# Optimization experiments

Measured on AMD Instinct MI355X. Metric: run time of the kernel, lower is better.

The kernel has to match this reference:

```python
import jax, jax.numpy as jnp
import numpy as np

H = 4096
NUM_HEADS = 32
D = 128
SEQ_LEN = 1024
CTX = 4096


def setup_inputs() -> dict:
    key = jax.random.key(0)
    k1, k2, k3, k4 = jax.random.split(key, 4)
    X = jax.random.normal(k1, (SEQ_LEN, H), dtype=jnp.float32)
    # Linear weight [out=3H, in=H]; scale ~1/sqrt(H) so attention logits are O(1)
    W = jax.random.normal(k2, (3 * H, H), dtype=jnp.float32) * (1.0 / np.sqrt(H))
    cache_K = jax.random.normal(k3, (1, CTX, NUM_HEADS, D), dtype=jnp.float32)
    cache_V = jax.random.normal(k4, (1, CTX, NUM_HEADS, D), dtype=jnp.float32)
    return {"X": X, "W": W, "cache_K": cache_K, "cache_V": cache_V}


def reference(X, W, cache_K, cache_V):
    seq_len, h = X.shape
    nh, d = cache_K.shape[2], cache_K.shape[3]
    # fused QKV projection (Linear, no bias): X @ W^T -> [seq_len, 3H]
    qkv = X @ W.T
    q, k, v = jnp.split(qkv, 3, axis=1)
    q = q.reshape(1, seq_len, nh, d)
    k = k.reshape(1, seq_len, nh, d)
    v = v.reshape(1, seq_len, nh, d)
    # concat KV cache along the sequence dim (cache_K[:, :P] with P = full cache)
    k_full = jnp.concatenate([cache_K, k], axis=1)  # [1, ctx+seq, nh, d]
    v_full = jnp.concatenate([cache_V, v], axis=1)
    scale = 1.0 / np.sqrt(d)
    # scores: [1, nh, seq_q, kv_len]
    scores = jnp.einsum("bqhd,bkhd->bhqk", q, k_full) * scale
    weights = jax.nn.softmax(scores, axis=-1)
    out = jnp.einsum("bhqk,bkhd->bqhd", weights, v_full)  # [1, seq, nh, d]
    return out.reshape(seq_len, h)
```

## Files before the change

kernel.cpp:

```cpp
#include <hip/hip_runtime.h>
#include <hip/hip_bf16.h>
#include <stdint.h>

#define H_DIM 4096
#define NH 32
#define HD 128
#define SEQ 1024
#define CTX 4096
#define KVL (CTX + SEQ)
#define W3H (3 * H_DIM)
#define ATTN_SCALE 0.08838834764831845f

typedef short short8 __attribute__((ext_vector_type(8)));
typedef float f32x4 __attribute__((ext_vector_type(4)));

#define GLOAD_LDS16(g, l)                                             \
  __builtin_amdgcn_global_load_lds(                                   \
      (const __attribute__((address_space(1))) void*)(g),             \
      (__attribute__((address_space(3))) void*)(l), 16, 0, 0)

__device__ __forceinline__ unsigned short f2b(float f) {
  union { float f; unsigned u; } v; v.f = f;
  return (unsigned short)((v.u + 0x7FFFu + ((v.u >> 16) & 1u)) >> 16);
}
__device__ __forceinline__ float b2f(unsigned short u) {
  union { unsigned u; float f; } v; v.u = ((unsigned)u) << 16;
  return v.f;
}

__global__ void k_cvt2(const float* __restrict__ X, const float* __restrict__ W,
                       unsigned short* __restrict__ Xb, unsigned short* __restrict__ Wb) {
  const int nx = SEQ * H_DIM / 4;
  const int nw = W3H * H_DIM / 4;
  int i = blockIdx.x * 256 + threadIdx.x;
  const float* s;
  unsigned short* d;
  int j;
  if (i < nx) { s = X; d = Xb; j = i; }
  else { j = i - nx; if (j >= nw) return; s = W; d = Wb; }
  float4 v = reinterpret_cast<const float4*>(s)[j];
  ushort4 o;
  o.x = f2b(v.x); o.y = f2b(v.y); o.z = f2b(v.z); o.w = f2b(v.w);
  reinterpret_cast<ushort4*>(d)[j] = o;
}

#define BM 128
#define BN 128
#define BK 64
__global__ __launch_bounds__(256, 2) void k_gemm_qkv(
    const unsigned short* __restrict__ A,
    const unsigned short* __restrict__ B,
    unsigned short* __restrict__ C) {
  __shared__ unsigned short As[BM * BK];
  __shared__ unsigned short Bs[BN * BK];
  const int tid = threadIdx.x;
  const int lane = tid & 63;
  const int wid = tid >> 6;
  const int bn = blockIdx.x, bm = blockIdx.y;
  const int wr = wid >> 1, wc = wid & 1;

  f32x4 acc[4][4] = {};

  const int lrow = lane >> 3;
  const int lcol = (lane & 7) * 8;
  const unsigned short* ga = A + (size_t)(bm * BM + wid * 32 + lrow) * H_DIM + lcol;
  const unsigned short* gb = B + (size_t)(bn * BN + wid * 32 + lrow) * H_DIM + lcol;

  for (int kt = 0; kt < H_DIM / BK; ++kt) {
    __syncthreads();
    const unsigned short* gak = ga + kt * BK;
    const unsigned short* gbk = gb + kt * BK;
#pragma unroll
    for (int i = 0; i < 4; ++i) {
      GLOAD_LDS16(gak + i * 8 * H_DIM, As + (wid * 4 + i) * 512);
      GLOAD_LDS16(gbk + i * 8 * H_DIM, Bs + (wid * 4 + i) * 512);
    }
    __syncthreads();
#pragma unroll
    for (int kk = 0; kk < 2; ++kk) {
      short8 af[4], bfr[4];
#pragma unroll
      for (int m = 0; m < 4; ++m)
        af[m] = *reinterpret_cast<const short8*>(
            As + (wr * 64 + m * 16 + (lane & 15)) * BK + kk * 32 + (lane >> 4) * 8);
#pragma unroll
      for (int n = 0; n < 4; ++n)
        bfr[n] = *reinterpret_cast<const short8*>(
            Bs + (wc * 64 + n * 16 + (lane & 15)) * BK + kk * 32 + (lane >> 4) * 8);
#pragma unroll
      for (int m = 0; m < 4; ++m)
#pragma unroll
        for (int n = 0; n < 4; ++n)
          acc[m][n] = __builtin_amdgcn_mfma_f32_16x16x32_bf16(af[m], bfr[n], acc[m][n], 0, 0, 0);
    }
  }
  const int r0 = bm * BM + wr * 64 + (lane >> 4) * 4;
  const int c0 = bn * BN + wc * 64 + (lane & 15);
#pragma unroll
  for (int m = 0; m < 4; ++m)
#pragma unroll
    for (int n = 0; n < 4; ++n)
#pragma unroll
      for (int r = 0; r < 4; ++r)
        C[(size_t)(r0 + m * 16 + r) * W3H + c0 + n * 16] = f2b(acc[m][n][r]);
}

__global__ void k_build_k(const float* __restrict__ cK, const unsigned short* __restrict__ QKV,
                          unsigned short* __restrict__ Kb) {
  int idx = (blockIdx.x * 256 + threadIdx.x) * 4;
  if (idx >= NH * KVL * HD) return;
  int h = idx / (KVL * HD);
  int rem = idx % (KVL * HD);
  int kv = rem / HD;
  int d = rem % HD;
  ushort4 o;
  if (kv < CTX) {
    float4 v = *reinterpret_cast<const float4*>(cK + ((size_t)kv * NH + h) * HD + d);
    o.x = f2b(v.x); o.y = f2b(v.y); o.z = f2b(v.z); o.w = f2b(v.w);
  } else {
    o = *reinterpret_cast<const ushort4*>(QKV + (size_t)(kv - CTX) * W3H + H_DIM + h * HD + d);
  }
  *reinterpret_cast<ushort4*>(Kb + idx) = o;
}

__global__ void k_build_vt(const float* __restrict__ cV, const unsigned short* __restrict__ QKV,
                           unsigned short* __restrict__ Vt) {
  __shared__ unsigned short T[HD][66];
  const int h = blockIdx.y;
  const int kt = blockIdx.x;
  const int t = threadIdx.x;
#pragma unroll
  for (int e = 0; e < 8; ++e) {
    int idx = (t + e * 256) * 4;
    int kvl = idx >> 7;
    int d = idx & 127;
    int kv = kt * 64 + kvl;
    unsigned short a, b, c, w;
    if (kv < CTX) {
      float4 v = *reinterpret_cast<const float4*>(cV + ((size_t)kv * NH + h) * HD + d);
      a = f2b(v.x); b = f2b(v.y); c = f2b(v.z); w = f2b(v.w);
    } else {
      ushort4 u = *reinterpret_cast<const ushort4*>(QKV + (size_t)(kv - CTX) * W3H + 2 * H_DIM + h * HD + d);
      a = u.x; b = u.y; c = u.z; w = u.w;
    }
    T[d][kvl] = a; T[d + 1][kvl] = b; T[d + 2][kvl] = c; T[d + 3][kvl] = w;
  }
  __syncthreads();
#pragma unroll
  for (int e = 0; e < 8; ++e) {
    int idx = (t + e * 256) * 4;
    int d = idx >> 6;
    int kv0 = idx & 63;
    ushort4 o;
    o.x = T[d][kv0]; o.y = T[d][kv0 + 1]; o.z = T[d][kv0 + 2]; o.w = T[d][kv0 + 3];
    *reinterpret_cast<ushort4*>(Vt + ((size_t)h * HD + d) * KVL + kt * 64 + kv0) = o;
  }
}

#define KVT 64
#define NT (KVL / KVT)
#define NT2 (NT / 2)
__global__ __launch_bounds__(256, 2) void k_attn(
    const unsigned short* __restrict__ QKV,
    const unsigned short* __restrict__ Kb,
    const unsigned short* __restrict__ Vt,
    float* __restrict__ A0,
    float* __restrict__ A1,
    float* __restrict__ Mp,
    float* __restrict__ Lp) {
  __shared__ unsigned short Ks[2][KVT * HD];
  __shared__ unsigned short Vs[2][KVT * HD];
  const int tid = threadIdx.x, lane = tid & 63, wid = tid >> 6;
  const int g = lane >> 4;
  const int qi = lane & 15;
  const int id = blockIdx.x;
  const int xcd = id & 7, slot = id >> 3;
  const int h = xcd * 4 + (slot >> 4);
  const int rem = slot & 15;
  const int qt = rem >> 1;
  const int split = rem & 1;
  const int kt0 = split * NT2;
  const int q0 = qt * 128 + wid * 32;

  short8 qf[2][4];
#pragma unroll
  for (int hf = 0; hf < 2; ++hf)
#pragma unroll
    for (int c = 0; c < 4; ++c) {
      short8 q = *reinterpret_cast<const short8*>(
          QKV + (size_t)(q0 + hf * 16 + qi) * W3H + h * HD + c * 32 + g * 8);
      short8 t;
#pragma unroll
      for (int j = 0; j < 8; ++j) t[j] = (short)f2b(b2f((unsigned short)q[j]) * ATTN_SCALE);
      qf[hf][c] = t;
    }

  float m_r[2] = {-1e30f, -1e30f}, l_r[2] = {0.f, 0.f};
  f32x4 acc_o[2][8] = {};

  const char* Kh = (const char*)(Kb + (size_t)h * KVL * HD);
  const char* Vh = (const char*)(Vt + (size_t)h * HD * KVL);

#define STAGE_K(t, b)                                                          \
  {                                                                            \
    _Pragma("unroll") for (int i = 0; i < 4; ++i) {                            \
      int c = wid * 4 + i;                                                     \
      int krow = c * 4 + (lane >> 4);                                          \
      int klcb = (16 * (lane & 15)) ^ ((krow & 7) << 4);                       \
      GLOAD_LDS16(Kh + (size_t)((t) * KVT + krow) * 256 + klcb,                \
                  (char*)Ks[b] + c * 1024);                                    \
    }                                                                          \
  }
#define STAGE_V(t, b)                                                          \
  {                                                                            \
    _Pragma("unroll") for (int i = 0; i < 4; ++i) {                            \
      int c = wid * 4 + i;                                                     \
      int vrow = c * 8 + (lane >> 3);                                          \
      int vlcb = (16 * (lane & 7)) ^ ((vrow & 7) << 4);                        \
      GLOAD_LDS16(Vh + (size_t)vrow * (KVL * 2) + (size_t)(t) * 128 + vlcb,    \
                  (char*)Vs[b] + c * 1024);                                    \
    }                                                                          \
  }
#define QKT(buf, S)                                                            \
  {                                                                            \
    _Pragma("unroll") for (int n = 0; n < 4; ++n) {                            \
      S[0][n] = (f32x4){0.f, 0.f, 0.f, 0.f};                                   \
      S[1][n] = (f32x4){0.f, 0.f, 0.f, 0.f};                                   \
    }                                                                          \
    __builtin_amdgcn_s_setprio(1);                                             \
    _Pragma("unroll") for (int n = 0; n < 4; ++n) {                            \
      int row = n * 16 + qi;                                                   \
      _Pragma("unroll") for (int c = 0; c < 4; ++c) {                          \
        int cb = (c * 32 + g * 8) * 2;                                         \
        short8 kf = *reinterpret_cast<const short8*>(                          \
            (const char*)Ks[buf] + row * 256 + (cb ^ ((row & 7) << 4)));       \
        S[0][n] = __builtin_amdgcn_mfma_f32_16x16x32_bf16(kf, qf[0][c], S[0][n], 0, 0, 0); \
        S[1][n] = __builtin_amdgcn_mfma_f32_16x16x32_bf16(kf, qf[1][c], S[1][n], 0, 0, 0); \
      }                                                                        \
    }                                                                          \
    __builtin_amdgcn_s_setprio(0);                                             \
  }

  const int i0 = ((2 * (g & 1) + 0) * 16 + qi) * 4;
  const int i1 = ((2 * (g & 1) + 1) * 16 + qi) * 4;

#define SMPV(S, vb)                                                            \
  {                                                                            \
    float p[2][4][4];                                                          \
    int okv = 1;                                                               \
    float tmax[2];                                                             \
    _Pragma("unroll") for (int hf = 0; hf < 2; ++hf) {                         \
      float t0 = S[hf][0][0];                                                  \
      _Pragma("unroll") for (int n = 0; n < 4; ++n)                            \
        _Pragma("unroll") for (int r = 0; r < 4; ++r)                          \
          t0 = fmaxf(t0, S[hf][n][r]);                                         \
      t0 = fmaxf(t0, __shfl_xor(t0, 16, 64));                                  \
      t0 = fmaxf(t0, __shfl_xor(t0, 32, 64));                                  \
      tmax[hf] = t0;                                                           \
      okv &= (t0 <= m_r[hf] + 8.0f);                                           \
    }                                                                          \
    if (!__all(okv)) {                                                         \
      _Pragma("unroll") for (int hf = 0; hf < 2; ++hf) {                       \
        float mn = fmaxf(m_r[hf], tmax[hf]);                                   \
        float alpha = __expf(m_r[hf] - mn);                                    \
        l_r[hf] *= alpha;                                                      \
        m_r[hf] = mn;                                                          \
        _Pragma("unroll") for (int nd = 0; nd < 8; ++nd) acc_o[hf][nd] *= alpha; \
      }                                                                        \
    }                                                                          \
    _Pragma("unroll") for (int hf = 0; hf < 2; ++hf) {                         \
      float sum = 0.f;                                                         \
      _Pragma("unroll") for (int n = 0; n < 4; ++n)                            \
        _Pragma("unroll") for (int r = 0; r < 4; ++r) {                        \
          p[hf][n][r] = __expf(S[hf][n][r] - m_r[hf]);                         \
          sum += p[hf][n][r];                                                  \
        }                                                                      \
      sum += __shfl_xor(sum, 16, 64);                                          \
      sum += __shfl_xor(sum, 32, 64);                                          \
      l_r[hf] += sum;                                                          \
    }                                                                          \
    unsigned pr[2][4][2];                                                      \
    _Pragma("unroll") for (int hf = 0; hf < 2; ++hf)                           \
      _Pragma("unroll") for (int n = 0; n < 4; ++n)                            \
        _Pragma("unroll") for (int rr = 0; rr < 2; ++rr) {                     \
          union { __hip_bfloat162 b; unsigned u; } cv;                         \
          cv.b = __float22bfloat162_rn(                                        \
              make_float2(p[hf][n][2 * rr], p[hf][n][2 * rr + 1]));            \
          pr[hf][n][rr] = cv.u;                                                \
        }                                                                      \
    _Pragma("unroll") for (int kc = 0; kc < 2; ++kc) {                         \
      short8 pv[2];                                                            \
      _Pragma("unroll") for (int hf = 0; hf < 2; ++hf) {                       \
        int a0 = __builtin_amdgcn_ds_bpermute(i0, (int)pr[hf][2 * kc][0]);     \
        int b0 = __builtin_amdgcn_ds_bpermute(i0, (int)pr[hf][2 * kc + 1][0]); \
        int a1 = __builtin_amdgcn_ds_bpermute(i0, (int)pr[hf][2 * kc][1]);     \
        int b1 = __builtin_amdgcn_ds_bpermute(i0, (int)pr[hf][2 * kc + 1][1]); \
        int a2 = __builtin_amdgcn_ds_bpermute(i1, (int)pr[hf][2 * kc][0]);     \
        int b2 = __builtin_amdgcn_ds_bpermute(i1, (int)pr[hf][2 * kc + 1][0]); \
        int a3 = __builtin_amdgcn_ds_bpermute(i1, (int)pr[hf][2 * kc][1]);     \
        int b3 = __builtin_amdgcn_ds_bpermute(i1, (int)pr[hf][2 * kc + 1][1]); \
        union { int i[4]; short8 s8; } u;                                      \
        u.i[0] = (g < 2) ? a0 : b0;                                            \
        u.i[1] = (g < 2) ? a1 : b1;                                            \
        u.i[2] = (g < 2) ? a2 : b2;                                            \
        u.i[3] = (g < 2) ? a3 : b3;                                            \
        pv[hf] = u.s8;                                                         \
      }                                                                        \
      __builtin_amdgcn_s_setprio(1);                                           \
      _Pragma("unroll") for (int nd = 0; nd < 8; ++nd) {                       \
        int row = nd * 16 + qi;                                                \
        int cb = kc * 64 + g * 16;                                             \
        short8 vf = *reinterpret_cast<const short8*>(                          \
            (const char*)Vs[vb] + row * 128 + (cb ^ ((row & 7) << 4)));        \
        acc_o[0][nd] = __builtin_amdgcn_mfma_f32_16x16x32_bf16(vf, pv[0], acc_o[0][nd], 0, 0, 0); \
        acc_o[1][nd] = __builtin_amdgcn_mfma_f32_16x16x32_bf16(vf, pv[1], acc_o[1][nd], 0, 0, 0); \
      }                                                                        \
      __builtin_amdgcn_s_setprio(0);                                           \
    }                                                                          \
  }

#define BODY(t, SC, SN)                                                        \
  {                                                                            \
    const int cur = (t) & 1;                                                   \
    if ((t) + 2 < NT2) STAGE_K(kt0 + (t) + 2, cur);                            \
    if ((t) + 1 < NT2) QKT(cur ^ 1, SN);                                       \
    SMPV(SC, cur);                                                             \
    __syncthreads();                                                           \
    if ((t) + 2 < NT2) STAGE_V(kt0 + (t) + 2, cur);                            \
  }

  STAGE_K(kt0, 0);
  STAGE_V(kt0, 0);
  STAGE_K(kt0 + 1, 1);
  STAGE_V(kt0 + 1, 1);
  __syncthreads();

  f32x4 sA[2][4], sB[2][4];
  QKT(0, sA);

  for (int tt = 0; tt < NT2; tt += 2) {
    BODY(tt, sA, sB);
    BODY(tt + 1, sB, sA);
  }

  float* Op = split ? A1 : A0;
#pragma unroll
  for (int hf = 0; hf < 2; ++hf) {
    float* orow = Op + (size_t)(q0 + hf * 16 + qi) * H_DIM + h * HD;
#pragma unroll
    for (int nd = 0; nd < 8; ++nd)
      *reinterpret_cast<float4*>(orow + nd * 16 + g * 4) =
          *reinterpret_cast<const float4*>(&acc_o[hf][nd]);
    if (g == 0) {
      int q = q0 + hf * 16 + qi;
      Mp[split * (NH * SEQ) + h * SEQ + q] = m_r[hf];
      Lp[split * (NH * SEQ) + h * SEQ + q] = l_r[hf];
    }
  }
#undef STAGE_K
#undef STAGE_V
#undef QKT
#undef SMPV
#undef BODY
}

__global__ void k_combine(const float* __restrict__ A1, const float* __restrict__ Mp,
                          const float* __restrict__ Lp, float* __restrict__ out) {
  int i4 = blockIdx.x * 256 + threadIdx.x;
  int q = i4 >> 10;
  int c4 = i4 & 1023;
  int h = c4 >> 5;
  float m0 = Mp[h * SEQ + q], m1 = Mp[NH * SEQ + h * SEQ + q];
  float l0 = Lp[h * SEQ + q], l1 = Lp[NH * SEQ + h * SEQ + q];
  float M = fmaxf(m0, m1);
  float w0 = __expf(m0 - M), w1 = __expf(m1 - M);
  float inv = 1.0f / (w0 * l0 + w1 * l1);
  float4 a0 = reinterpret_cast<const float4*>(out)[i4];
  float4 a1 = reinterpret_cast<const float4*>(A1)[i4];
  float4 o;
  o.x = (w0 * a0.x + w1 * a1.x) * inv;
  o.y = (w0 * a0.y + w1 * a1.y) * inv;
  o.z = (w0 * a0.z + w1 * a1.z) * inv;
  o.w = (w0 * a0.w + w1 * a1.w) * inv;
  reinterpret_cast<float4*>(out)[i4] = o;
}

extern "C" void kernel_launch(void* const* d_in, const int* in_sizes, int n_in,
                              void* d_out, int out_size, void* d_ws, size_t ws_size,
                              hipStream_t stream) {
  const float* X = (const float*)d_in[0];
  const float* W = (const float*)d_in[1];
  const float* cK = (const float*)d_in[2];
  const float* cV = (const float*)d_in[3];
  float* out = (float*)d_out;
  char* ws = (char*)d_ws;

  unsigned short* Xb = (unsigned short*)(ws);
  float* Mp = (float*)(ws);
  float* Lp = (float*)(ws + (256 << 10));
  unsigned short* QKVb = (unsigned short*)(ws + ((size_t)8 << 20));
  unsigned short* Wb = (unsigned short*)(ws + ((size_t)32 << 20));
  unsigned short* Kb = (unsigned short*)(ws + ((size_t)32 << 20));
  unsigned short* Vt = (unsigned short*)(ws + ((size_t)72 << 20));
  float* A1 = (float*)(ws + ((size_t)112 << 20));

  int ncvt = (SEQ * H_DIM + W3H * H_DIM) / 4;
  k_cvt2<<<(ncvt + 255) / 256, 256, 0, stream>>>(X, W, Xb, Wb);

  dim3 gg(W3H / BN, SEQ / BM);
  k_gemm_qkv<<<gg, 256, 0, stream>>>(Xb, Wb, QKVb);

  k_build_k<<<(NH * KVL * HD / 4) / 256, 256, 0, stream>>>(cK, QKVb, Kb);
  dim3 gv(KVL / 64, NH);
  k_build_vt<<<gv, 256, 0, stream>>>(cV, QKVb, Vt);

  k_attn<<<SEQ / 128 * NH * 2, 256, 0, stream>>>(QKVb, Kb, Vt, out, A1, Mp, Lp);
  k_combine<<<(SEQ * H_DIM / 4) / 256, 256, 0, stream>>>(A1, Mp, Lp, out);
}
```

Baseline: 354.4 us.

## Rewrite QKV GEMM with 256x256 tiles, double-buffered LDS and XOR swizzle

The QKV projection GEMM moves from 128x128 tiles with a single LDS buffer to 256x256 tiles on 512 threads. It double-buffers 128KB of LDS so global-to-LDS loads of the next k-tiles overlap the MFMA work, and XOR-swizzles the LDS layout to avoid bank conflicts. It also remaps block IDs for L2 locality and raises wave priority around the MFMA bursts. The cost is 192 blocks on a 256-CU part, which leaves some CUs idle, plus heavy LDS use and register pressure from 32 accumulators per thread.

```diff
diff --git a/kernel.cpp b/kernel.cpp
--- a/kernel.cpp
+++ b/kernel.cpp
@@ -44,65 +44,101 @@
   reinterpret_cast<ushort4*>(d)[j] = o;
 }
 
-#define BM 128
-#define BN 128
-#define BK 64
-__global__ __launch_bounds__(256, 2) void k_gemm_qkv(
+#define GBM 256
+#define GBN 256
+#define GBK 64
+#define GNKT (H_DIM / GBK)
+__global__ __launch_bounds__(512, 2) void k_gemm_qkv(
     const unsigned short* __restrict__ A,
     const unsigned short* __restrict__ B,
     unsigned short* __restrict__ C) {
-  __shared__ unsigned short As[BM * BK];
-  __shared__ unsigned short Bs[BN * BK];
+  __shared__ __align__(16) char Lds[131072];
   const int tid = threadIdx.x;
   const int lane = tid & 63;
   const int wid = tid >> 6;
-  const int bn = blockIdx.x, bm = blockIdx.y;
-  const int wr = wid >> 1, wc = wid & 1;
-
-  f32x4 acc[4][4] = {};
-
-  const int lrow = lane >> 3;
-  const int lcol = (lane & 7) * 8;
-  const unsigned short* ga = A + (size_t)(bm * BM + wid * 32 + lrow) * H_DIM + lcol;
-  const unsigned short* gb = B + (size_t)(bn * BN + wid * 32 + lrow) * H_DIM + lcol;
-
-  for (int kt = 0; kt < H_DIM / BK; ++kt) {
-    __syncthreads();
-    const unsigned short* gak = ga + kt * BK;
-    const unsigned short* gbk = gb + kt * BK;
-#pragma unroll
-    for (int i = 0; i < 4; ++i) {
-      GLOAD_LDS16(gak + i * 8 * H_DIM, As + (wid * 4 + i) * 512);
-      GLOAD_LDS16(gbk + i * 8 * H_DIM, Bs + (wid * 4 + i) * 512);
+  const int wm = wid >> 2;
+  const int wn = wid & 3;
+  const int lq = lane >> 4;
+  const int lr = lane & 15;
+
+  const int id = blockIdx.x;
+  const int wg = (id & 7) * 24 + (id >> 3);
+  const int bm = wg & 3;
+  const int bn = wg >> 2;
+
+  const int sel = 8 * ((lane & 7) ^ (lane >> 3));
+
+#define GSTAGE(t, buf)                                                         \
+  {                                                                            \
+    _Pragma("unroll") for (int i = 0; i < 4; ++i) {                            \
+      int c = wid * 4 + i;                                                     \
+      GLOAD_LDS16(A + (size_t)(bm * GBM + c * 8 + (lane >> 3)) * H_DIM +       \
+                      (t) * GBK + sel,                                         \
+                  Lds + (buf) * 65536 + c * 1024);                             \
+      GLOAD_LDS16(B + (size_t)(bn * GBN + c * 8 + (lane >> 3)) * H_DIM +       \
+                      (t) * GBK + sel,                                         \
+                  Lds + (buf) * 65536 + 32768 + c * 1024);                     \
+    }                                                                          \
+  }
+
+  f32x4 acc[8][4] = {};
+
+#define GCOMP(buf)                                                             \
+  {                                                                            \
+    _Pragma("unroll") for (int kk = 0; kk < 2; ++kk) {                         \
+      short8 af[8], bfr[4];                                                    \
+      _Pragma("unroll") for (int m = 0; m < 8; ++m)                            \
+        af[m] = *reinterpret_cast<const short8*>(                              \
+            Lds + (buf) * 65536 + (wm * 128 + m * 16 + lr) * 128 +             \
+            16 * ((kk * 4 + lq) ^ (lr & 7)));                                  \
+      _Pragma("unroll") for (int n = 0; n < 4; ++n)                            \
+        bfr[n] = *reinterpret_cast<const short8*>(                             \
+            Lds + (buf) * 65536 + 32768 + (wn * 64 + n * 16 + lr) * 128 +      \
+            16 * ((kk * 4 + lq) ^ (lr & 7)));                                  \
+      __builtin_amdgcn_s_setprio(1);                                           \
+      _Pragma("unroll") for (int m = 0; m < 8; ++m)                            \
+        _Pragma("unroll") for (int n = 0; n < 4; ++n)                          \
+          acc[m][n] = __builtin_amdgcn_mfma_f32_16x16x32_bf16(                 \
+              af[m], bfr[n], acc[m][n], 0, 0, 0);                              \
+      __builtin_amdgcn_s_setprio(0);                                           \
+    }                                                                          \
+  }
+
+  GSTAGE(0, 0);
+  GSTAGE(1, 1);
+  asm volatile("s_waitcnt vmcnt(8)" ::: "memory");
+  __builtin_amdgcn_sched_barrier(0);
+  __builtin_amdgcn_s_barrier();
+  __builtin_amdgcn_sched_barrier(0);
+
+  for (int t = 0; t < GNKT; ++t) {
+    const int cur = t & 1;
+    GCOMP(cur);
+    __builtin_amdgcn_sched_barrier(0);
+    __builtin_amdgcn_s_barrier();
+    __builtin_amdgcn_sched_barrier(0);
+    if (t + 2 < GNKT) {
+      GSTAGE(t + 2, cur);
+      asm volatile("s_waitcnt vmcnt(8)" ::: "memory");
+    } else {
+      asm volatile("s_waitcnt vmcnt(0)" ::: "memory");
     }
-    __syncthreads();
-#pragma unroll
-    for (int kk = 0; kk < 2; ++kk) {
-      short8 af[4], bfr[4];
-#pragma unroll
-      for (int m = 0; m < 4; ++m)
-        af[m] = *reinterpret_cast<const short8*>(
-            As + (wr * 64 + m * 16 + (lane & 15)) * BK + kk * 32 + (lane >> 4) * 8);
-#pragma unroll
-      for (int n = 0; n < 4; ++n)
-        bfr[n] = *reinterpret_cast<const short8*>(
-            Bs + (wc * 64 + n * 16 + (lane & 15)) * BK + kk * 32 + (lane >> 4) * 8);
-#pragma unroll
-      for (int m = 0; m < 4; ++m)
-#pragma unroll
-        for (int n = 0; n < 4; ++n)
-          acc[m][n] = __builtin_amdgcn_mfma_f32_16x16x32_bf16(af[m], bfr[n], acc[m][n], 0, 0, 0);
-    }
-  }
-  const int r0 = bm * BM + wr * 64 + (lane >> 4) * 4;
-  const int c0 = bn * BN + wc * 64 + (lane & 15);
-#pragma unroll
-  for (int m = 0; m < 4; ++m)
+    __builtin_amdgcn_sched_barrier(0);
+    __builtin_amdgcn_s_barrier();
+    __builtin_amdgcn_sched_barrier(0);
+  }
+
+  const int r0 = bm * GBM + wm * 128 + lq * 4;
+  const int c0 = bn * GBN + wn * 64 + lr;
+#pragma unroll
+  for (int m = 0; m < 8; ++m)
 #pragma unroll
     for (int n = 0; n < 4; ++n)
 #pragma unroll
       for (int r = 0; r < 4; ++r)
         C[(size_t)(r0 + m * 16 + r) * W3H + c0 + n * 16] = f2b(acc[m][n][r]);
+#undef GSTAGE
+#undef GCOMP
 }
 
 __global__ void k_build_k(const float* __restrict__ cK, const unsigned short* __restrict__ QKV,
@@ -407,8 +443,7 @@
   int ncvt = (SEQ * H_DIM + W3H * H_DIM) / 4;
   k_cvt2<<<(ncvt + 255) / 256, 256, 0, stream>>>(X, W, Xb, Wb);
 
-  dim3 gg(W3H / BN, SEQ / BM);
-  k_gemm_qkv<<<gg, 256, 0, stream>>>(Xb, Wb, QKVb);
+  k_gemm_qkv<<<(SEQ / GBM) * (W3H / GBN), 512, 0, stream>>>(Xb, Wb, QKVb);
 
   k_build_k<<<(NH * KVL * HD / 4) / 256, 256, 0, stream>>>(cK, QKVb, Kb);
   dim3 gv(KVL / 64, NH);
```

Measured after the change: 359.5 us. About the same (+1.4%).
